# Optimization experiments

Measured on AMD Instinct MI355X. Metric: run time of the kernel, lower is better.

The kernel has to match this reference:

```python
import jax, jax.numpy as jnp
import numpy as np

N_GT = 8192
N_PRED = 8192
DIM = 3
EDGE_PROB = 6.0 / N_PRED  # sparse mesh-like adjacency, avg degree ~6


def setup_inputs() -> dict:
    key = jax.random.key(0)
    k1, k2, k3, k4 = jax.random.split(key, 4)
    preds = jax.random.normal(k1, (N_PRED, DIM), dtype=jnp.float32)
    gts = jax.random.normal(k2, (N_GT, DIM), dtype=jnp.float32)
    gts_normals = jax.random.normal(k3, (N_GT, DIM), dtype=jnp.float32)
    # binary float adjacency matrix, as in the torch module (A cast to FloatTensor)
    A = (jax.random.uniform(k4, (N_PRED, N_PRED)) < EDGE_PROB).astype(jnp.float32)
    return {"preds": preds, "gts": gts, "gts_normals": gts_normals, "A": A}


def reference(preds, gts, gts_normals, A):
    # --- batch_pairwise_dist(gts, preds): P[i, j] = ||gts_i - preds_j||^2 ---
    # (N_gt, N_pred); computed via the same rx + ry - 2*zz expansion
    P = (
        jnp.sum(gts * gts, axis=1)[:, None]
        + jnp.sum(preds * preds, axis=1)[None, :]
        - 2.0 * gts @ preds.T
    )
    nearest_gt = jnp.argmin(P, axis=0)          # (N_pred,) index into gts
    q = gts_normals[nearest_gt]                  # (N_pred, 3) nearest-neighbor normals

    # --- normal_pred + calculate_loss, fused ---
    # Original builds x_diff[d, i, j] = (preds[i, d] - preds[j, d]) * A[i, j]
    # then inner[i, j] = sum_d q[j, d] * x_diff[d, i, j], loss = sum(inner^2).
    # Equivalent without the (3, N, N) tensor:
    #   dot[i, j] = preds[i] . q[j] - preds[j] . q[j]
    dot = preds @ q.T - jnp.sum(preds * q, axis=1)[None, :]  # (N_pred, N_pred)
    inner = dot * A
    return jnp.sum(inner * inner)
```

## Files before the change

### kernel.cpp

```cpp
#include <hip/hip_runtime.h>

#define N 8192
#define NN_BLOCKS 512
#define SCAN_BLOCKS 2048
#define SCAN_THREADS (SCAN_BLOCKS * 256)
#define QUADS (N * (N / 4))
#define SLOT_CAP 256
#define GCHUNK 1024


__global__ __launch_bounds__(256) void combined_kernel(
        const float* __restrict__ preds,
        const float* __restrict__ gts,
        const float* __restrict__ gn,
        float4* __restrict__ qpq,
        const float4* __restrict__ A4,
        unsigned int* __restrict__ cnt,
        uint2* __restrict__ hits,
        float* __restrict__ out) {
    __shared__ float sgf[GCHUNK * 3];
    __shared__ unsigned int scnt;

    const int tid = threadIdx.x;

    if (blockIdx.x < NN_BLOCKS) {
        if (blockIdx.x == 0 && tid == 0) out[0] = 0.0f;

        const int lane = tid & 63;
        const int wv   = tid >> 6;
        const int j0   = blockIdx.x * 16 + wv * 4;

        float px[4], py[4], pz[4], bestV[4];
        int bestI[4];
        #pragma unroll
        for (int k = 0; k < 4; ++k) {
            px[k] = preds[(j0 + k) * 3 + 0];
            py[k] = preds[(j0 + k) * 3 + 1];
            pz[k] = preds[(j0 + k) * 3 + 2];
            bestV[k] = 3.4e38f;
            bestI[k] = 0;
        }

        for (int c = 0; c < N / GCHUNK; ++c) {
            #pragma unroll
            for (int s = 0; s < GCHUNK * 3 / 256; ++s) {
                const int t = s * 256 + tid;
                sgf[t] = gts[c * GCHUNK * 3 + t];
            }
            __syncthreads();

            #pragma unroll 4
            for (int it = 0; it < GCHUNK / 64; ++it) {
                const int t  = it * 64 + lane;
                const float gx = sgf[t * 3 + 0];
                const float gy = sgf[t * 3 + 1];
                const float gz = sgf[t * 3 + 2];
                float gg = gx * gx;
                gg = fmaf(gy, gy, gg);
                gg = fmaf(gz, gz, gg);
                const int gi = c * GCHUNK + t;
                #pragma unroll
                for (int k = 0; k < 4; ++k) {
                    float d = gx * px[k];
                    d = fmaf(gy, py[k], d);
                    d = fmaf(gz, pz[k], d);
                    const float v = fmaf(-2.0f, d, gg);
                    if (v < bestV[k]) { bestV[k] = v; bestI[k] = gi; }
                }
            }
            __syncthreads();
        }

        #pragma unroll
        for (int d = 1; d < 64; d <<= 1) {
            #pragma unroll
            for (int k = 0; k < 4; ++k) {
                const float ov = __shfl_xor(bestV[k], d);
                const int   oi = __shfl_xor(bestI[k], d);
                if (ov < bestV[k] || (ov == bestV[k] && oi < bestI[k])) {
                    bestV[k] = ov; bestI[k] = oi;
                }
            }
        }

        if (lane == 0) {
            #pragma unroll
            for (int k = 0; k < 4; ++k) {
                const int bi = bestI[k];
                const float qx = gn[bi * 3 + 0];
                const float qy = gn[bi * 3 + 1];
                const float qz = gn[bi * 3 + 2];
                const float pq = px[k] * qx + py[k] * qy + pz[k] * qz;
                qpq[j0 + k] = make_float4(qx, qy, qz, pq);
            }
        }
    } else {
        if (tid == 0) scnt = 0u;
        __syncthreads();

        const int sb   = blockIdx.x - NN_BLOCKS;
        const int base = sb * 256 + tid;
        uint2* slot = hits + (size_t)sb * SLOT_CAP;

        #pragma unroll 1
        for (int g = 0; g < QUADS / SCAN_THREADS / 4; ++g) {
            int u[4];
            float4 a[4];
            #pragma unroll
            for (int k = 0; k < 4; ++k) {
                u[k] = base + (g * 4 + k) * SCAN_THREADS;
                a[k] = A4[u[k]];
            }
            #pragma unroll
            for (int k = 0; k < 4; ++k) {
                if (a[k].x != 0.0f || a[k].y != 0.0f ||
                    a[k].z != 0.0f || a[k].w != 0.0f) {
                    const unsigned int i  = (unsigned)(u[k] >> 11);
                    const unsigned int j0 = (unsigned)((u[k] & 2047) << 2);
                    const float av[4] = { a[k].x, a[k].y, a[k].z, a[k].w };
                    #pragma unroll
                    for (int c = 0; c < 4; ++c) {
                        if (av[c] != 0.0f) {
                            const unsigned int p = atomicAdd(&scnt, 1u);
                            if (p < SLOT_CAP) {
                                slot[p] = make_uint2((i << 13) | (j0 + c),
                                                     __float_as_uint(av[c]));
                            }
                        }
                    }
                }
            }
        }

        __syncthreads();
        if (tid == 0) cnt[sb] = scnt < SLOT_CAP ? scnt : SLOT_CAP;
    }
}

__global__ __launch_bounds__(256) void loss_kernel(
        const float* __restrict__ preds,
        const float4* __restrict__ qpq,
        const unsigned int* __restrict__ cnt,
        const uint2* __restrict__ hits,
        float* __restrict__ out) {
    const int lane    = threadIdx.x & 63;
    const int wave_id = blockIdx.x * 4 + (threadIdx.x >> 6);
    float sum = 0.0f;

    #pragma unroll
    for (int s = 0; s < 4; ++s) {
        const int sb = wave_id * 4 + s;
        const unsigned int c = cnt[sb];
        const uint2* slot = hits + (size_t)sb * SLOT_CAP;
        for (unsigned int t = lane; t < c; t += 64) {
            const uint2 h = slot[t];
            const unsigned int i = h.x >> 13;
            const unsigned int j = h.x & 8191u;
            const float av = __uint_as_float(h.y);
            const float4 q = qpq[j];
            float d = preds[i * 3 + 0] * q.x;
            d = fmaf(preds[i * 3 + 1], q.y, d);
            d = fmaf(preds[i * 3 + 2], q.z, d);
            d = (d - q.w) * av;
            sum = fmaf(d, d, sum);
        }
    }

    #pragma unroll
    for (int d = 32; d > 0; d >>= 1) sum += __shfl_down(sum, d);

    __shared__ float wsum[4];
    if (lane == 0) wsum[threadIdx.x >> 6] = sum;
    __syncthreads();
    if (threadIdx.x == 0) {
        atomicAdd(out, wsum[0] + wsum[1] + wsum[2] + wsum[3]);
    }
}

extern "C" void kernel_launch(void* const* d_in, const int* in_sizes, int n_in,
                              void* d_out, int out_size, void* d_ws, size_t ws_size,
                              hipStream_t stream) {
    const float* preds = (const float*)d_in[0];
    const float* gts   = (const float*)d_in[1];
    const float* gn    = (const float*)d_in[2];
    const float* A     = (const float*)d_in[3];
    float* out = (float*)d_out;

    char* ws = (char*)d_ws;
    float4*       qpq  = (float4*)(ws);
    unsigned int* cnt  = (unsigned int*)(ws + 131072);
    uint2*        hits = (uint2*)(ws + 139264);

    combined_kernel<<<NN_BLOCKS + SCAN_BLOCKS, 256, 0, stream>>>(
        preds, gts, gn, qpq, (const float4*)A, cnt, hits, out);
    loss_kernel<<<128, 256, 0, stream>>>(preds, qpq, cnt, hits, out);
}
```

Before: 54.59 us.

## Split adjacency scan across all blocks, including NN blocks, with contiguous chunks

The adjacency scan is redistributed so the nearest-neighbour blocks also scan a share of A once their search finishes, and the scan-only block count drops from 2048 to 1536. Each block now reads contiguous 512-quad chunks instead of grid-strided quads. Hits are staged in shared memory and copied to global at the end. The aim is to balance the bandwidth-bound scan against the compute-bound NN search in one grid, at the cost of NN blocks running longer, and the loss kernel's slot count (2048) must still match the grid size.

```diff
diff --git a/kernel.cpp b/kernel.cpp
--- a/kernel.cpp
+++ b/kernel.cpp
@@ -1,15 +1,20 @@
 #include <hip/hip_runtime.h>
 
 #define N 8192
-#define NN_BLOCKS 512
-#define SCAN_BLOCKS 2048
-#define SCAN_THREADS (SCAN_BLOCKS * 256)
-#define QUADS (N * (N / 4))
+#define NNB 512
+#define SCB 1536
+#define GRID_B (NNB + SCB)
+#define CQUADS 512
+#define NCHUNKS (N * (N / 4) / CQUADS)
+#define NN_CH 13
+#define SC_CH 17
 #define SLOT_CAP 256
 #define GCHUNK 1024
 
-
-__global__ __launch_bounds__(256) void combined_kernel(
+static_assert(NNB * NN_CH + SCB * SC_CH == NCHUNKS, "chunk split must cover A");
+
+
+__global__ __launch_bounds__(256) void fused_kernel(
         const float* __restrict__ preds,
         const float* __restrict__ gts,
         const float* __restrict__ gn,
@@ -18,17 +23,19 @@
         unsigned int* __restrict__ cnt,
         uint2* __restrict__ hits,
         float* __restrict__ out) {
-    __shared__ float sgf[GCHUNK * 3];
+    __shared__ __align__(16) float sgf[GCHUNK * 3];
     __shared__ unsigned int scnt;
 
     const int tid = threadIdx.x;
-
-    if (blockIdx.x < NN_BLOCKS) {
-        if (blockIdx.x == 0 && tid == 0) out[0] = 0.0f;
+    const int b   = blockIdx.x;
+
+    int ch0, nch;
+    if (b < NNB) {
+        if (b == 0 && tid == 0) out[0] = 0.0f;
 
         const int lane = tid & 63;
         const int wv   = tid >> 6;
-        const int j0   = blockIdx.x * 16 + wv * 4;
+        const int j0   = b * 16 + wv * 4;
 
         float px[4], py[4], pz[4], bestV[4];
         int bestI[4];
@@ -94,47 +101,51 @@
                 qpq[j0 + k] = make_float4(qx, qy, qz, pq);
             }
         }
+
+        ch0 = b * NN_CH;
+        nch = NN_CH;
     } else {
-        if (tid == 0) scnt = 0u;
-        __syncthreads();
-
-        const int sb   = blockIdx.x - NN_BLOCKS;
-        const int base = sb * 256 + tid;
-        uint2* slot = hits + (size_t)sb * SLOT_CAP;
-
-        #pragma unroll 1
-        for (int g = 0; g < QUADS / SCAN_THREADS / 4; ++g) {
-            int u[4];
-            float4 a[4];
-            #pragma unroll
-            for (int k = 0; k < 4; ++k) {
-                u[k] = base + (g * 4 + k) * SCAN_THREADS;
-                a[k] = A4[u[k]];
-            }
-            #pragma unroll
-            for (int k = 0; k < 4; ++k) {
-                if (a[k].x != 0.0f || a[k].y != 0.0f ||
-                    a[k].z != 0.0f || a[k].w != 0.0f) {
-                    const unsigned int i  = (unsigned)(u[k] >> 11);
-                    const unsigned int j0 = (unsigned)((u[k] & 2047) << 2);
-                    const float av[4] = { a[k].x, a[k].y, a[k].z, a[k].w };
-                    #pragma unroll
-                    for (int c = 0; c < 4; ++c) {
-                        if (av[c] != 0.0f) {
-                            const unsigned int p = atomicAdd(&scnt, 1u);
-                            if (p < SLOT_CAP) {
-                                slot[p] = make_uint2((i << 13) | (j0 + c),
-                                                     __float_as_uint(av[c]));
-                            }
+        ch0 = NNB * NN_CH + (b - NNB) * SC_CH;
+        nch = SC_CH;
+    }
+
+    if (tid == 0) scnt = 0u;
+    __syncthreads();
+
+    uint2* hbuf = (uint2*)sgf;
+    uint2* slot = hits + (size_t)b * SLOT_CAP;
+
+    for (int cc = 0; cc < nch; ++cc) {
+        const int base = (ch0 + cc) * CQUADS + tid;
+        const float4 a0 = A4[base];
+        const float4 a1 = A4[base + 256];
+
+        #pragma unroll
+        for (int h = 0; h < 2; ++h) {
+            const float4 a = h ? a1 : a0;
+            const int u = h ? (base + 256) : base;
+            if (a.x != 0.0f || a.y != 0.0f || a.z != 0.0f || a.w != 0.0f) {
+                const unsigned int i  = (unsigned)(u >> 11);
+                const unsigned int j0 = (unsigned)((u & 2047) << 2);
+                const float av[4] = { a.x, a.y, a.z, a.w };
+                #pragma unroll
+                for (int c = 0; c < 4; ++c) {
+                    if (av[c] != 0.0f) {
+                        const unsigned int p = atomicAdd(&scnt, 1u);
+                        if (p < SLOT_CAP) {
+                            hbuf[p] = make_uint2((i << 13) | (j0 + c),
+                                                 __float_as_uint(av[c]));
                         }
                     }
                 }
             }
         }
-
-        __syncthreads();
-        if (tid == 0) cnt[sb] = scnt < SLOT_CAP ? scnt : SLOT_CAP;
-    }
+    }
+
+    __syncthreads();
+    const unsigned int n = scnt < SLOT_CAP ? scnt : SLOT_CAP;
+    for (unsigned int t = tid; t < n; t += 256) slot[t] = hbuf[t];
+    if (tid == 0) cnt[b] = n;
 }
 
 __global__ __launch_bounds__(256) void loss_kernel(
@@ -150,7 +161,7 @@
     #pragma unroll
     for (int s = 0; s < 4; ++s) {
         const int sb = wave_id * 4 + s;
-        const unsigned int c = cnt[sb];
+        const unsigned int c = cnt[sb] < SLOT_CAP ? cnt[sb] : SLOT_CAP;
         const uint2* slot = hits + (size_t)sb * SLOT_CAP;
         for (unsigned int t = lane; t < c; t += 64) {
             const uint2 h = slot[t];
@@ -191,7 +202,7 @@
     unsigned int* cnt  = (unsigned int*)(ws + 131072);
     uint2*        hits = (uint2*)(ws + 139264);
 
-    combined_kernel<<<NN_BLOCKS + SCAN_BLOCKS, 256, 0, stream>>>(
+    fused_kernel<<<GRID_B, 256, 0, stream>>>(
         preds, gts, gn, qpq, (const float4*)A, cnt, hits, out);
     loss_kernel<<<128, 256, 0, stream>>>(preds, qpq, cnt, hits, out);
 }
```

New measurement: 50.05 us (median of 2 runs). -8.3%, faster.
